# Optimization experiments

Hardware: AMD Instinct MI355X
Metric: run time of the kernel (lower is better)

The kernel has to match this reference:

```python
import jax, jax.numpy as jnp
import numpy as np

N_HEADS = 4  # top-k experts per token (init arg n_heads)


def setup_inputs() -> dict:
    key = jax.random.key(0)
    k1, k2, k3, k4 = jax.random.split(key, 4)
    dmodel, n_experts, expert_size = 1024, 64, 128
    B, S = 4, 2048
    x = jax.random.normal(k1, (B, S, dmodel), dtype=jnp.float32)
    # init stds follow the module: sel ~ d^-0.5, keys ~ d^-0.5, values ~ (n_experts*expert_size)^-0.5
    expert_sel = jax.random.normal(k2, (n_experts, dmodel), dtype=jnp.float32) * (dmodel ** -0.5)
    keys = jax.random.normal(k3, (n_experts, dmodel, expert_size), dtype=jnp.float32) * (dmodel ** -0.5)
    values = jax.random.normal(k4, (n_experts, expert_size, dmodel), dtype=jnp.float32) * ((n_experts * expert_size) ** -0.5)
    return {"x": x, "expert_sel": expert_sel, "keys": keys, "values": values}


def reference(x, expert_sel, keys, values):
    B, S, d = x.shape
    n_experts = keys.shape[0]
    xf = x.reshape(-1, d)                               # [N, d]
    N = xf.shape[0]
    # expert selection: sigmoid gates, top-k experts per token
    logits = xf @ expert_sel.T                           # [N, K]
    sel = jax.nn.sigmoid(logits)
    sel_val, sel_idx = jax.lax.top_k(sel, N_HEADS)       # [N, H]
    # dense gate mask: gate[n,k] = sigmoid gate if expert k selected else 0
    gates = jnp.zeros((N, n_experts), dtype=x.dtype)
    gates = gates.at[jnp.arange(N)[:, None], sel_idx].set(sel_val)
    # per-expert key projection + ReLU + gate (relu(0)*0 == 0 so dense-masked form is exact)
    h = jnp.einsum('nd,kde->nke', xf, keys)              # [N, K, E]
    scores = jax.nn.relu(h) * gates[:, :, None]
    # weighted gather-sum over per-expert values (embedding_bag mode='sum')
    out = jnp.einsum('nke,kev->nv', scores, values)      # [N, v_dim]
    return out.reshape(B, S, -1)
```

## Files before the change

kernel.cpp:

```cpp
#include <hip/hip_runtime.h>

typedef __bf16 bf16x8 __attribute__((ext_vector_type(8)));
typedef float f32x4 __attribute__((ext_vector_type(4)));

#define N_TOK 8192
#define DMODEL 1024
#define NEXP 64
#define ESIZE 128
#define WL_MAX 576

__device__ __forceinline__ unsigned short f2bf(float f) {
  unsigned int u = __builtin_bit_cast(unsigned int, f);
  u += 0x7FFFu + ((u >> 16) & 1u);
  return (unsigned short)(u >> 16);
}

__device__ __forceinline__ float b2f(unsigned short u) {
  unsigned int v = ((unsigned int)u) << 16;
  return __builtin_bit_cast(float, v);
}

__device__ __forceinline__ void gld16(unsigned short* lds, const unsigned short* g) {
  __builtin_amdgcn_global_load_lds(
      (const __attribute__((address_space(1))) unsigned int*)g,
      (__attribute__((address_space(3))) unsigned int*)lds, 16, 0, 0);
}

__global__ void k_split2(const float* __restrict__ x, unsigned short* __restrict__ xh,
                         unsigned short* __restrict__ xl, const float* __restrict__ esel,
                         unsigned short* __restrict__ sh_, unsigned short* __restrict__ sl_,
                         int* __restrict__ zeroPtr) {
  if (blockIdx.x == 0 && threadIdx.x < 128) zeroPtr[threadIdx.x] = 0;
  size_t gid = (size_t)blockIdx.x * 256 + threadIdx.x;
  const size_t NX = (size_t)N_TOK * DMODEL / 8;
  const float* in;
  unsigned short *ho, *lo2;
  size_t i;
  if (gid < NX) {
    in = x; ho = xh; lo2 = xl; i = gid * 8;
  } else {
    in = esel; ho = sh_; lo2 = sl_; i = (gid - NX) * 8;
  }
  float4 a = *reinterpret_cast<const float4*>(in + i);
  float4 b = *reinterpret_cast<const float4*>(in + i + 4);
  unsigned short h[8], l[8];
  float v[8] = {a.x, a.y, a.z, a.w, b.x, b.y, b.z, b.w};
#pragma unroll
  for (int q = 0; q < 8; ++q) {
    h[q] = f2bf(v[q]);
    l[q] = f2bf(v[q] - b2f(h[q]));
  }
  uint4 oh, ol;
  oh.x = h[0] | ((unsigned)h[1] << 16); oh.y = h[2] | ((unsigned)h[3] << 16);
  oh.z = h[4] | ((unsigned)h[5] << 16); oh.w = h[6] | ((unsigned)h[7] << 16);
  ol.x = l[0] | ((unsigned)l[1] << 16); ol.y = l[2] | ((unsigned)l[3] << 16);
  ol.z = l[4] | ((unsigned)l[5] << 16); ol.w = l[6] | ((unsigned)l[7] << 16);
  *reinterpret_cast<uint4*>(ho + i) = oh;
  *reinterpret_cast<uint4*>(lo2 + i) = ol;
}

__global__ void k_transpose2(const float* __restrict__ keys, unsigned short* __restrict__ kout,
                             const float* __restrict__ values, unsigned short* __restrict__ vout) {
  __shared__ float t[32][33];
  const float* in;
  unsigned short* out;
  int R, C;
  if (blockIdx.z == 0) { in = keys; out = kout; R = DMODEL; C = ESIZE; }
  else { in = values; out = vout; R = ESIZE; C = DMODEL; }
  int b = blockIdx.y;
  int tilesC = C >> 5;
  int tr = blockIdx.x / tilesC, tc = blockIdx.x % tilesC;
  int lr = threadIdx.x >> 5, lc = threadIdx.x & 31;
  const float* ip = in + (size_t)b * R * C;
  unsigned short* op = out + (size_t)b * R * C;
#pragma unroll
  for (int p = 0; p < 4; ++p)
    t[p * 8 + lr][lc] = ip[(size_t)(tr * 32 + p * 8 + lr) * C + tc * 32 + lc];
  __syncthreads();
#pragma unroll
  for (int p = 0; p < 4; ++p)
    op[(size_t)(tc * 32 + p * 8 + lr) * R + tr * 32 + lc] = f2bf(t[lc][p * 8 + lr]);
}

__global__ __launch_bounds__(256) void k_rlogit(const unsigned short* __restrict__ xh,
                                                const unsigned short* __restrict__ xl,
                                                const unsigned short* __restrict__ sh,
                                                const unsigned short* __restrict__ sl,
                                                int4* __restrict__ idx4,
                                                float4* __restrict__ g4,
                                                int* __restrict__ gcount,
                                                int* __restrict__ glist) {
  int tid = threadIdx.x, lane = tid & 63;
  int tok0 = blockIdx.x * 32;
  int wv = tid >> 6, wr = wv >> 1, wc = wv & 1;
  int cc = lane & 15, grp = lane >> 4;

  __shared__ alignas(16) unsigned short stage[24576];
  __shared__ float lg[32][68];

  int arow = tid >> 3, ach = tid & 7;
  int swz = (ach ^ (arow & 7)) * 8;
  const unsigned short* srcAh = xh + (size_t)(tok0 + arow) * DMODEL + swz;
  const unsigned short* srcAl = xl + (size_t)(tok0 + arow) * DMODEL + swz;
  const unsigned short* srcBh0 = sh + (size_t)arow * DMODEL + swz;
  const unsigned short* srcBh1 = sh + (size_t)(32 + arow) * DMODEL + swz;
  const unsigned short* srcBl0 = sl + (size_t)arow * DMODEL + swz;
  const unsigned short* srcBl1 = sl + (size_t)(32 + arow) * DMODEL + swz;

  auto stg = [&](int bo , int kk) {
    unsigned short* s = stage + bo;
    gld16(s + tid * 8, srcAh + kk);
    gld16(s + 2048 + tid * 8, srcAl + kk);
    gld16(s + 4096 + tid * 8, srcBh0 + kk);
    gld16(s + 6144 + tid * 8, srcBh1 + kk);
    gld16(s + 8192 + tid * 8, srcBl0 + kk);
    gld16(s + 10240 + tid * 8, srcBl1 + kk);
  };

  f32x4 acc[2] = {};
  stg(0, 0);
  __syncthreads();
  const char* sb = (const char*)stage;
  int ra = wr * 16 + cc;
  int rb0 = wc * 32 + cc, rb1 = wc * 32 + 16 + cc;
  for (int t = 0; t < 16; ++t) {
    int curB = (t & 1) * 24576;
    if (t < 15) stg(((t + 1) & 1) * 12288, (t + 1) * 64);
#pragma unroll
    for (int ks = 0; ks < 2; ++ks) {
      int o_a = (((ks * 4 + grp) ^ (ra & 7)) * 16);
      bf16x8 aH = *reinterpret_cast<const bf16x8*>(sb + curB + ra * 128 + o_a);
      bf16x8 aL = *reinterpret_cast<const bf16x8*>(sb + curB + 4096 + ra * 128 + o_a);
      int o_b0 = (((ks * 4 + grp) ^ (rb0 & 7)) * 16);
      int o_b1 = (((ks * 4 + grp) ^ (rb1 & 7)) * 16);
      bf16x8 bH0 = *reinterpret_cast<const bf16x8*>(sb + curB + 8192 + rb0 * 128 + o_b0);
      bf16x8 bH1 = *reinterpret_cast<const bf16x8*>(sb + curB + 8192 + rb1 * 128 + o_b1);
      bf16x8 bL0 = *reinterpret_cast<const bf16x8*>(sb + curB + 16384 + rb0 * 128 + o_b0);
      bf16x8 bL1 = *reinterpret_cast<const bf16x8*>(sb + curB + 16384 + rb1 * 128 + o_b1);
      acc[0] = __builtin_amdgcn_mfma_f32_16x16x32_bf16(aH, bH0, acc[0], 0, 0, 0);
      acc[0] = __builtin_amdgcn_mfma_f32_16x16x32_bf16(aH, bL0, acc[0], 0, 0, 0);
      acc[0] = __builtin_amdgcn_mfma_f32_16x16x32_bf16(aL, bH0, acc[0], 0, 0, 0);
      acc[1] = __builtin_amdgcn_mfma_f32_16x16x32_bf16(aH, bH1, acc[1], 0, 0, 0);
      acc[1] = __builtin_amdgcn_mfma_f32_16x16x32_bf16(aH, bL1, acc[1], 0, 0, 0);
      acc[1] = __builtin_amdgcn_mfma_f32_16x16x32_bf16(aL, bH1, acc[1], 0, 0, 0);
    }
    __syncthreads();
  }

#pragma unroll
  for (int n = 0; n < 2; ++n)
#pragma unroll
    for (int r = 0; r < 4; ++r)
      lg[wr * 16 + grp * 4 + r][wc * 32 + n * 16 + cc] = acc[n][r];
  __syncthreads();

  if (tid < 32) {
    float bv0 = -3e38f, bv1 = -3e38f, bv2 = -3e38f, bv3 = -3e38f, bv4 = -3e38f;
    int bi0 = 0, bi1 = 0, bi2 = 0, bi3 = 0;
    for (int e = 0; e < 64; ++e) {
      float v = lg[tid][e];
      if (v > bv4) {
        if (v > bv0) {
          bv4 = bv3; bv3 = bv2; bi3 = bi2; bv2 = bv1; bi2 = bi1; bv1 = bv0; bi1 = bi0; bv0 = v; bi0 = e;
        } else if (v > bv1) {
          bv4 = bv3; bv3 = bv2; bi3 = bi2; bv2 = bv1; bi2 = bi1; bv1 = v; bi1 = e;
        } else if (v > bv2) {
          bv4 = bv3; bv3 = bv2; bi3 = bi2; bv2 = v; bi2 = e;
        } else if (v > bv3) {
          bv4 = bv3; bv3 = v; bi3 = e;
        } else {
          bv4 = v;
        }
      }
    }
    idx4[tok0 + tid] = make_int4(bi0, bi1, bi2, bi3);
    float4 g;
    g.x = 1.0f / (1.0f + __expf(-bv0));
    g.y = 1.0f / (1.0f + __expf(-bv1));
    g.z = 1.0f / (1.0f + __expf(-bv2));
    g.w = 1.0f / (1.0f + __expf(-bv3));
    g4[tok0 + tid] = g;
    if (bv3 - bv4 < 1e-4f) {
      int p = atomicAdd(gcount, 1);
      glist[p] = tok0 + tid;
    }
  }
}

__global__ __launch_bounds__(256) void k_refine(const float* __restrict__ x,
                                                const float* __restrict__ esel,
                                                const int* __restrict__ gcount,
                                                const int* __restrict__ glist,
                                                int4* __restrict__ idx4,
                                                float4* __restrict__ g4) {
  __shared__ double lp[256];
  __shared__ double lgt[64];
  int cnt = *gcount;
  for (int i = blockIdx.x; i < cnt; i += 64) {
    int n = glist[i];
    int e = threadIdx.x & 63, jq = threadIdx.x >> 6;
    const float* xr = x + (size_t)n * DMODEL + jq * 256;
    const float* er = esel + (size_t)e * DMODEL + jq * 256;
    double s = 0.0;
    for (int j = 0; j < 256; ++j)
      s += (double)xr[j] * (double)er[j];
    lp[threadIdx.x] = s;
    __syncthreads();
    if (threadIdx.x < 64)
      lgt[threadIdx.x] =
          lp[threadIdx.x] + lp[64 + threadIdx.x] + lp[128 + threadIdx.x] + lp[192 + threadIdx.x];
    __syncthreads();
    if (threadIdx.x == 0) {
      double bv0 = -1.0e300, bv1 = -1.0e300, bv2 = -1.0e300, bv3 = -1.0e300;
      int bi0 = 0, bi1 = 0, bi2 = 0, bi3 = 0;
      for (int e2 = 0; e2 < 64; ++e2) {
        double v = lgt[e2];
        if (v > bv3) {
          if (v > bv0) {
            bv3 = bv2; bi3 = bi2; bv2 = bv1; bi2 = bi1; bv1 = bv0; bi1 = bi0; bv0 = v; bi0 = e2;
          } else if (v > bv1) {
            bv3 = bv2; bi3 = bi2; bv2 = bv1; bi2 = bi1; bv1 = v; bi1 = e2;
          } else if (v > bv2) {
            bv3 = bv2; bi3 = bi2; bv2 = v; bi2 = e2;
          } else {
            bv3 = v; bi3 = e2;
          }
        }
      }
      idx4[n] = make_int4(bi0, bi1, bi2, bi3);
      float4 g;
      g.x = 1.0f / (1.0f + __expf(-(float)bv0));
      g.y = 1.0f / (1.0f + __expf(-(float)bv1));
      g.z = 1.0f / (1.0f + __expf(-(float)bv2));
      g.w = 1.0f / (1.0f + __expf(-(float)bv3));
      g4[n] = g;
    }
    __syncthreads();
  }
}

__global__ __launch_bounds__(256) void k_bucket(const int4* __restrict__ idx4,
                                                const float4* __restrict__ g4,
                                                int* __restrict__ btok,
                                                float* __restrict__ bgate,
                                                int* __restrict__ cnt) {
  __shared__ int lcnt[64];
  __shared__ int lbase[64];
  int tid = threadIdx.x;
  if (tid < 64) lcnt[tid] = 0;
  __syncthreads();
  int n = blockIdx.x * 256 + tid;
  int4 I = idx4[n];
  float4 G = g4[n];
  int e[4] = {I.x, I.y, I.z, I.w};
  float g[4] = {G.x, G.y, G.z, G.w};
  int pos[4];
#pragma unroll
  for (int h = 0; h < 4; ++h) pos[h] = atomicAdd(&lcnt[e[h]], 1);
  __syncthreads();
  if (tid < 64 && lcnt[tid] > 0) lbase[tid] = atomicAdd(&cnt[tid], lcnt[tid]);
  __syncthreads();
#pragma unroll
  for (int h = 0; h < 4; ++h) {
    int slot = lbase[e[h]] + pos[h];
    btok[e[h] * N_TOK + slot] = h * N_TOK + n;
    bgate[e[h] * N_TOK + slot] = g[h];
  }
}

__global__ void k_worklist(const int* __restrict__ cnt, int* __restrict__ wl) {
  int lane = threadIdx.x;
  int nt = (cnt[lane] + 63) >> 6;
  int off = nt;
  for (int d = 1; d < 64; d <<= 1) {
    int o = __shfl_up(off, d);
    if (lane >= d) off += o;
  }
  int total = __shfl(off, 63);
  off -= nt;
  for (int t = 0; t < nt; ++t) wl[off + t] = (lane << 8) | t;
  for (int i = total + lane; i < WL_MAX; i += 64) wl[i] = -1;
}

__global__ __launch_bounds__(512, 4) void k_expert(
    const unsigned short* __restrict__ xbf, const unsigned short* __restrict__ kbf,
    const unsigned short* __restrict__ vbf, const int* __restrict__ wl,
    const int* __restrict__ btok, const float* __restrict__ bgate,
    const int* __restrict__ cnt, unsigned short* __restrict__ part) {
  int wid = (blockIdx.x & 7) * (WL_MAX / 8) + (blockIdx.x >> 3);
  int wle = wl[wid];
  if (wle < 0) return;
  int k = wle >> 8, tile = wle & 255;
  int ck = cnt[k];
  int tid = threadIdx.x, lane = tid & 63;
  int wv = tid >> 6, wr = wv >> 2, wc = wv & 3;
  int cc = lane & 15, grp = lane >> 4;

  __shared__ alignas(16) unsigned short stage[24576];
  __shared__ alignas(16) unsigned short lS[64 * 136];
  __shared__ int sRow[64];
  __shared__ float sGate[64];

  if (tid < 64) {
    int i = tile * 64 + tid;
    bool valid = i < ck;
    sRow[tid] = valid ? btok[k * N_TOK + i] : 4 * N_TOK + wid;
    sGate[tid] = valid ? bgate[k * N_TOK + i] : 0.0f;
  }
  __syncthreads();

  const unsigned short* kb = kbf + (size_t)k * (ESIZE * DMODEL);
  const unsigned short* vb = vbf + (size_t)k * (DMODEL * ESIZE);
  char* sbase = (char*)stage;

  int arow = tid >> 3, ach = tid & 7;
  const unsigned short* srcA =
      xbf + (size_t)(sRow[arow] & (N_TOK - 1)) * DMODEL + ((ach ^ (arow & 7)) * 8);
  int b1row = 64 + arow;
  const unsigned short* srcB0 = kb + (size_t)arow * DMODEL + ((ach ^ (arow & 7)) * 8);
  const unsigned short* srcB1 = kb + (size_t)b1row * DMODEL + ((ach ^ (b1row & 7)) * 8);

  auto stg1 = [&](int boB, int kk) {
    unsigned short* s = (unsigned short*)(sbase + boB);
    gld16(s + tid * 8, srcA + kk);
    gld16(s + 4096 + tid * 8, srcB0 + kk);
    gld16(s + 8192 + tid * 8, srcB1 + kk);
  };

  f32x4 acc[2][2] = {};
  stg1(0, 0);
  __syncthreads();
  for (int t = 0; t < 16; ++t) {
    int curB = (t & 1) * 24576;
    if (t < 15) stg1(((t + 1) & 1) * 24576, (t + 1) * 64);
    bf16x8 aF[2][2], bF[2][2];
#pragma unroll
    for (int ks = 0; ks < 2; ++ks) {
#pragma unroll
      for (int m = 0; m < 2; ++m) {
        int r = wr * 32 + m * 16 + cc;
        aF[ks][m] = *reinterpret_cast<const bf16x8*>(
            sbase + curB + r * 128 + (((ks * 4 + grp) ^ (r & 7)) * 16));
      }
#pragma unroll
      for (int n = 0; n < 2; ++n) {
        int r = wc * 32 + n * 16 + cc;
        bF[ks][n] = *reinterpret_cast<const bf16x8*>(
            sbase + curB + 8192 + r * 128 + (((ks * 4 + grp) ^ (r & 7)) * 16));
      }
    }
#pragma unroll
    for (int ks = 0; ks < 2; ++ks)
#pragma unroll
      for (int m = 0; m < 2; ++m)
#pragma unroll
        for (int n = 0; n < 2; ++n)
          acc[m][n] = __builtin_amdgcn_mfma_f32_16x16x32_bf16(aF[ks][m], bF[ks][n], acc[m][n], 0, 0, 0);
    __syncthreads();
  }

  int v0row = tid >> 4, vch = tid & 15;
  int v1row = 32 + v0row;
  const unsigned short* srcV0 = vb + (size_t)v0row * ESIZE + ((vch ^ (v0row & 15)) * 8);
  const unsigned short* srcV1 = vb + (size_t)v1row * ESIZE + ((vch ^ (v1row & 15)) * 8);
  auto stgV = [&](int boB, int ch) {
    unsigned short* s = (unsigned short*)(sbase + boB);
    const size_t co = (size_t)ch * 64 * ESIZE;
    gld16(s + tid * 8, srcV0 + co);
    gld16(s + 4096 + tid * 8, srcV1 + co);
  };

  stgV(0, 0);

#pragma unroll
  for (int m = 0; m < 2; ++m) {
    int trow = wr * 32 + m * 16 + grp * 4;
#pragma unroll
    for (int n = 0; n < 2; ++n) {
      int e = wc * 32 + n * 16 + cc;
#pragma unroll
      for (int r = 0; r < 4; ++r) {
        float s = acc[m][n][r];
        s = s > 0.0f ? s * sGate[trow + r] : 0.0f;
        lS[(trow + r) * 136 + e] = f2bf(s);
      }
    }
  }
  __syncthreads();

  bf16x8 sF[2][4];
#pragma unroll
  for (int m = 0; m < 2; ++m) {
    int r = wr * 32 + m * 16 + cc;
#pragma unroll
    for (int ks = 0; ks < 4; ++ks)
      sF[m][ks] = *reinterpret_cast<const bf16x8*>((const char*)lS + r * 272 + ks * 64 + grp * 16);
  }
  unsigned short* rB[2][4];
#pragma unroll
  for (int m = 0; m < 2; ++m)
#pragma unroll
    for (int r = 0; r < 4; ++r)
      rB[m][r] = part + (size_t)sRow[wr * 32 + m * 16 + grp * 4 + r] * DMODEL + wc * 16 + cc;

  for (int ch = 0; ch < 16; ++ch) {
    int curB = (ch & 1) * 16384;
    if (ch < 15) stgV(((ch + 1) & 1) * 16384, ch + 1);
    int r = wc * 16 + cc;
    bf16x8 vF[4];
#pragma unroll
    for (int ks = 0; ks < 4; ++ks)
      vF[ks] = *reinterpret_cast<const bf16x8*>(
          sbase + curB + r * 256 + (((ks * 4 + grp) ^ cc) * 16));
    f32x4 o[2] = {};
#pragma unroll
    for (int ks = 0; ks < 4; ++ks)
#pragma unroll
      for (int m = 0; m < 2; ++m)
        o[m] = __builtin_amdgcn_mfma_f32_16x16x32_bf16(sF[m][ks], vF[ks], o[m], 0, 0, 0);
#pragma unroll
    for (int m = 0; m < 2; ++m)
#pragma unroll
      for (int r2 = 0; r2 < 4; ++r2)
        rB[m][r2][ch * 64] = f2bf(o[m][r2]);
    __syncthreads();
  }
}

__global__ void k_sum(const unsigned short* __restrict__ part, float* __restrict__ out) {
  size_t i = ((size_t)blockIdx.x * 256 + threadIdx.x) * 8;
  const size_t stride = (size_t)N_TOK * DMODEL;
  uint4 a = *reinterpret_cast<const uint4*>(part + i);
  uint4 b = *reinterpret_cast<const uint4*>(part + stride + i);
  uint4 c = *reinterpret_cast<const uint4*>(part + 2 * stride + i);
  uint4 d = *reinterpret_cast<const uint4*>(part + 3 * stride + i);
  float o[8];
#pragma unroll
  for (int q = 0; q < 4; ++q) {
    unsigned ua = (&a.x)[q], ub = (&b.x)[q], uc = (&c.x)[q], ud = (&d.x)[q];
    o[q * 2 + 0] = b2f((unsigned short)ua) + b2f((unsigned short)ub) +
                   b2f((unsigned short)uc) + b2f((unsigned short)ud);
    o[q * 2 + 1] = b2f((unsigned short)(ua >> 16)) + b2f((unsigned short)(ub >> 16)) +
                   b2f((unsigned short)(uc >> 16)) + b2f((unsigned short)(ud >> 16));
  }
  *reinterpret_cast<float4*>(out + i) = make_float4(o[0], o[1], o[2], o[3]);
  *reinterpret_cast<float4*>(out + i + 4) = make_float4(o[4], o[5], o[6], o[7]);
}

extern "C" void kernel_launch(void* const* d_in, const int* in_sizes, int n_in,
                              void* d_out, int out_size, void* d_ws, size_t ws_size,
                              hipStream_t stream) {
  const float* x = (const float*)d_in[0];
  const float* esel = (const float*)d_in[1];
  const float* keys = (const float*)d_in[2];
  const float* values = (const float*)d_in[3];
  float* out = (float*)d_out;

  char* p = (char*)d_ws;
  unsigned short* xbf = (unsigned short*)p; p += (size_t)N_TOK * DMODEL * 2;
  unsigned short* xlo = (unsigned short*)p; p += (size_t)N_TOK * DMODEL * 2;
  unsigned short* kbf = (unsigned short*)p; p += (size_t)NEXP * DMODEL * ESIZE * 2;
  unsigned short* vbf = (unsigned short*)p; p += (size_t)NEXP * DMODEL * ESIZE * 2;
  unsigned short* selbh = (unsigned short*)p; p += (size_t)NEXP * DMODEL * 2;
  unsigned short* selbl = (unsigned short*)p; p += (size_t)NEXP * DMODEL * 2;
  float4* g4 = (float4*)p; p += (size_t)N_TOK * 16;
  int4* idx4 = (int4*)p; p += (size_t)N_TOK * 16;
  int* btok = (int*)p; p += (size_t)NEXP * N_TOK * 4;
  float* bgate = (float*)p; p += (size_t)NEXP * N_TOK * 4;
  unsigned short* part = (unsigned short*)p;
  p += ((size_t)4 * N_TOK + WL_MAX) * DMODEL * 2;
  int* cnt = (int*)p; p += 256;
  int* gcount = (int*)p; p += 256;
  int* wl = (int*)p; p += WL_MAX * 4;
  int* glist = (int*)p; p += N_TOK * 4;
  (void)ws_size; (void)in_sizes; (void)n_in;

  const int splitBlocks = (int)(((size_t)N_TOK * DMODEL + (size_t)NEXP * DMODEL) / 8 / 256);
  k_split2<<<splitBlocks, 256, 0, stream>>>(x, xbf, xlo, esel, selbh, selbl, cnt);
  k_transpose2<<<dim3(128, 64, 2), 256, 0, stream>>>(keys, kbf, values, vbf);
  k_rlogit<<<256, 256, 0, stream>>>(xbf, xlo, selbh, selbl, idx4, g4, gcount, glist);
  k_refine<<<64, 256, 0, stream>>>(x, esel, gcount, glist, idx4, g4);
  k_bucket<<<32, 256, 0, stream>>>(idx4, g4, btok, bgate, cnt);
  k_worklist<<<1, 64, 0, stream>>>(cnt, wl);
  k_expert<<<WL_MAX, 512, 0, stream>>>(xbf, kbf, vbf, wl, btok, bgate, cnt, part);
  k_sum<<<(N_TOK * DMODEL / 8) / 256, 256, 0, stream>>>(part, out);
}
```

Measured before the change: 152.9 us.

## Merge split and transpose prep kernels; alias score buffer into LDS stage

Fuses the bf16 hi/lo split kernel and the keys/values transpose kernel into one launch, selecting the path by block index, which removes one kernel launch and the gap between them. In k_expert the gated-score tile is moved into the stage LDS buffer, with the V double buffer shifted to offset 17408 so it does not overlap the scores. This cuts per-block LDS use, and the launch bound minimum is raised from 4 to 6 blocks to target higher occupancy. The risk is register spilling under the tighter launch bound.

```diff
diff --git a/kernel.cpp b/kernel.cpp
--- a/kernel.cpp
+++ b/kernel.cpp
@@ -8,6 +8,7 @@
 #define NEXP 64
 #define ESIZE 128
 #define WL_MAX 576
+#define PREP_SPLIT 4128
 
 __device__ __forceinline__ unsigned short f2bf(float f) {
   unsigned int u = __builtin_bit_cast(unsigned int, f);
@@ -26,51 +27,54 @@
       (__attribute__((address_space(3))) unsigned int*)lds, 16, 0, 0);
 }
 
-__global__ void k_split2(const float* __restrict__ x, unsigned short* __restrict__ xh,
-                         unsigned short* __restrict__ xl, const float* __restrict__ esel,
-                         unsigned short* __restrict__ sh_, unsigned short* __restrict__ sl_,
-                         int* __restrict__ zeroPtr) {
-  if (blockIdx.x == 0 && threadIdx.x < 128) zeroPtr[threadIdx.x] = 0;
-  size_t gid = (size_t)blockIdx.x * 256 + threadIdx.x;
-  const size_t NX = (size_t)N_TOK * DMODEL / 8;
-  const float* in;
-  unsigned short *ho, *lo2;
-  size_t i;
-  if (gid < NX) {
-    in = x; ho = xh; lo2 = xl; i = gid * 8;
-  } else {
-    in = esel; ho = sh_; lo2 = sl_; i = (gid - NX) * 8;
-  }
-  float4 a = *reinterpret_cast<const float4*>(in + i);
-  float4 b = *reinterpret_cast<const float4*>(in + i + 4);
-  unsigned short h[8], l[8];
-  float v[8] = {a.x, a.y, a.z, a.w, b.x, b.y, b.z, b.w};
-#pragma unroll
-  for (int q = 0; q < 8; ++q) {
-    h[q] = f2bf(v[q]);
-    l[q] = f2bf(v[q] - b2f(h[q]));
-  }
-  uint4 oh, ol;
-  oh.x = h[0] | ((unsigned)h[1] << 16); oh.y = h[2] | ((unsigned)h[3] << 16);
-  oh.z = h[4] | ((unsigned)h[5] << 16); oh.w = h[6] | ((unsigned)h[7] << 16);
-  ol.x = l[0] | ((unsigned)l[1] << 16); ol.y = l[2] | ((unsigned)l[3] << 16);
-  ol.z = l[4] | ((unsigned)l[5] << 16); ol.w = l[6] | ((unsigned)l[7] << 16);
-  *reinterpret_cast<uint4*>(ho + i) = oh;
-  *reinterpret_cast<uint4*>(lo2 + i) = ol;
-}
-
-__global__ void k_transpose2(const float* __restrict__ keys, unsigned short* __restrict__ kout,
-                             const float* __restrict__ values, unsigned short* __restrict__ vout) {
+__global__ void k_prep(const float* __restrict__ x, unsigned short* __restrict__ xh,
+                       unsigned short* __restrict__ xl, const float* __restrict__ esel,
+                       unsigned short* __restrict__ sh_, unsigned short* __restrict__ sl_,
+                       const float* __restrict__ keys, unsigned short* __restrict__ kout,
+                       const float* __restrict__ values, unsigned short* __restrict__ vout,
+                       int* __restrict__ zeroPtr) {
   __shared__ float t[32][33];
+  int bid = blockIdx.x, tid = threadIdx.x;
+  if (bid < PREP_SPLIT) {
+    if (bid == 0 && tid < 128) zeroPtr[tid] = 0;
+    size_t gid = (size_t)bid * 256 + tid;
+    const size_t NX = (size_t)N_TOK * DMODEL / 8;
+    const float* in;
+    unsigned short *ho, *lo2;
+    size_t i;
+    if (gid < NX) {
+      in = x; ho = xh; lo2 = xl; i = gid * 8;
+    } else {
+      in = esel; ho = sh_; lo2 = sl_; i = (gid - NX) * 8;
+    }
+    float4 a = *reinterpret_cast<const float4*>(in + i);
+    float4 b = *reinterpret_cast<const float4*>(in + i + 4);
+    unsigned short h[8], l[8];
+    float v[8] = {a.x, a.y, a.z, a.w, b.x, b.y, b.z, b.w};
+#pragma unroll
+    for (int q = 0; q < 8; ++q) {
+      h[q] = f2bf(v[q]);
+      l[q] = f2bf(v[q] - b2f(h[q]));
+    }
+    uint4 oh, ol;
+    oh.x = h[0] | ((unsigned)h[1] << 16); oh.y = h[2] | ((unsigned)h[3] << 16);
+    oh.z = h[4] | ((unsigned)h[5] << 16); oh.w = h[6] | ((unsigned)h[7] << 16);
+    ol.x = l[0] | ((unsigned)l[1] << 16); ol.y = l[2] | ((unsigned)l[3] << 16);
+    ol.z = l[4] | ((unsigned)l[5] << 16); ol.w = l[6] | ((unsigned)l[7] << 16);
+    *reinterpret_cast<uint4*>(ho + i) = oh;
+    *reinterpret_cast<uint4*>(lo2 + i) = ol;
+    return;
+  }
+  int tt = bid - PREP_SPLIT;
   const float* in;
   unsigned short* out;
   int R, C;
-  if (blockIdx.z == 0) { in = keys; out = kout; R = DMODEL; C = ESIZE; }
-  else { in = values; out = vout; R = ESIZE; C = DMODEL; }
-  int b = blockIdx.y;
+  if (tt < 8192) { in = keys; out = kout; R = DMODEL; C = ESIZE; }
+  else { in = values; out = vout; R = ESIZE; C = DMODEL; tt -= 8192; }
+  int b = tt >> 7, tile = tt & 127;
   int tilesC = C >> 5;
-  int tr = blockIdx.x / tilesC, tc = blockIdx.x % tilesC;
-  int lr = threadIdx.x >> 5, lc = threadIdx.x & 31;
+  int tr = tile / tilesC, tc = tile % tilesC;
+  int lr = tid >> 5, lc = tid & 31;
   const float* ip = in + (size_t)b * R * C;
   unsigned short* op = out + (size_t)b * R * C;
 #pragma unroll
@@ -282,7 +286,7 @@
   for (int i = total + lane; i < WL_MAX; i += 64) wl[i] = -1;
 }
 
-__global__ __launch_bounds__(512, 4) void k_expert(
+__global__ __launch_bounds__(512, 6) void k_expert(
     const unsigned short* __restrict__ xbf, const unsigned short* __restrict__ kbf,
     const unsigned short* __restrict__ vbf, const int* __restrict__ wl,
     const int* __restrict__ btok, const float* __restrict__ bgate,
@@ -296,8 +300,7 @@
   int wv = tid >> 6, wr = wv >> 2, wc = wv & 3;
   int cc = lane & 15, grp = lane >> 4;
 
-  __shared__ alignas(16) unsigned short stage[24576];
-  __shared__ alignas(16) unsigned short lS[64 * 136];
+  __shared__ alignas(16) unsigned short stage[25088];
   __shared__ int sRow[64];
   __shared__ float sGate[64];
 
@@ -370,7 +373,7 @@
     gld16(s + 4096 + tid * 8, srcV1 + co);
   };
 
-  stgV(0, 0);
+  stgV(17408, 0);
 
 #pragma unroll
   for (int m = 0; m < 2; ++m) {
@@ -382,7 +385,7 @@
       for (int r = 0; r < 4; ++r) {
         float s = acc[m][n][r];
         s = s > 0.0f ? s * sGate[trow + r] : 0.0f;
-        lS[(trow + r) * 136 + e] = f2bf(s);
+        stage[(trow + r) * 136 + e] = f2bf(s);
       }
     }
   }
@@ -394,7 +397,7 @@
     int r = wr * 32 + m * 16 + cc;
 #pragma unroll
     for (int ks = 0; ks < 4; ++ks)
-      sF[m][ks] = *reinterpret_cast<const bf16x8*>((const char*)lS + r * 272 + ks * 64 + grp * 16);
+      sF[m][ks] = *reinterpret_cast<const bf16x8*>((const char*)stage + r * 272 + ks * 64 + grp * 16);
   }
   unsigned short* rB[2][4];
 #pragma unroll
@@ -404,8 +407,8 @@
       rB[m][r] = part + (size_t)sRow[wr * 32 + m * 16 + grp * 4 + r] * DMODEL + wc * 16 + cc;
 
   for (int ch = 0; ch < 16; ++ch) {
-    int curB = (ch & 1) * 16384;
-    if (ch < 15) stgV(((ch + 1) & 1) * 16384, ch + 1);
+    int curB = 17408 + (ch & 1) * 16384;
+    if (ch < 15) stgV(17408 + (((ch + 1) & 1) * 16384), ch + 1);
     int r = wc * 16 + cc;
     bf16x8 vF[4];
 #pragma unroll
@@ -475,9 +478,8 @@
   int* glist = (int*)p; p += N_TOK * 4;
   (void)ws_size; (void)in_sizes; (void)n_in;
 
-  const int splitBlocks = (int)(((size_t)N_TOK * DMODEL + (size_t)NEXP * DMODEL) / 8 / 256);
-  k_split2<<<splitBlocks, 256, 0, stream>>>(x, xbf, xlo, esel, selbh, selbl, cnt);
-  k_transpose2<<<dim3(128, 64, 2), 256, 0, stream>>>(keys, kbf, values, vbf);
+  k_prep<<<PREP_SPLIT + 16384, 256, 0, stream>>>(x, xbf, xlo, esel, selbh, selbl,
+                                                 keys, kbf, values, vbf, cnt);
   k_rlogit<<<256, 256, 0, stream>>>(xbf, xlo, selbh, selbl, idx4, g4, gcount, glist);
   k_refine<<<64, 256, 0, stream>>>(x, esel, gcount, glist, idx4, g4);
   k_bucket<<<32, 256, 0, stream>>>(idx4, g4, btok, bgate, cnt);
```

New measurement: 137.8 us. 1.11x faster.
